# Kernel tuning notes

Hardware: AMD Instinct MI355X
Metric: run time of the kernel (lower is better)

## Reference

```python
import jax, jax.numpy as jnp
import numpy as np

N = 100_000      # nodes
E = 1_600_000    # edges (avg degree 16)
D_IN = 256
D_OUT = 128


def setup_inputs() -> dict:
    key = jax.random.key(0)
    ks = jax.random.split(key, 13)
    stdv = 1.0 / np.sqrt(D_OUT)      # matches reset_parameters
    std_att = 1.0                    # att_vec_* have fan 1 -> stdv 1
    std_av = 1.0 / np.sqrt(3.0)
    return {
        "x": jax.random.normal(ks[0], (N, D_IN), dtype=jnp.float32),
        "edge_src": jax.random.randint(ks[1], (E,), 0, N),
        "edge_dst": jax.random.randint(ks[2], (E,), 0, N),
        "w_low": jax.random.uniform(ks[3], (E,), dtype=jnp.float32) / 16.0,   # ~normalized adj
        "w_high": jax.random.normal(ks[4], (E,), dtype=jnp.float32) / 16.0,    # high-pass weights can be +/-
        "w_unnorm": jax.random.uniform(ks[5], (E,), dtype=jnp.float32),
        "W_low": jax.random.uniform(ks[6], (D_IN, D_OUT), jnp.float32, -stdv, stdv),
        "W_high": jax.random.uniform(ks[7], (D_IN, D_OUT), jnp.float32, -stdv, stdv),
        "W_mlp": jax.random.uniform(ks[8], (D_IN, D_OUT), jnp.float32, -stdv, stdv),
        "a_low": jax.random.uniform(ks[9], (D_OUT, 1), jnp.float32, -std_att, std_att),
        "a_high": jax.random.uniform(ks[10], (D_OUT, 1), jnp.float32, -std_att, std_att),
        "a_mlp": jax.random.uniform(ks[11], (D_OUT, 1), jnp.float32, -std_att, std_att),
        "att_vec": jax.random.uniform(ks[12], (3, 3), jnp.float32, -std_av, std_av),
    }


def _spmm(w, src, dst, h, n):
    # sparse [n,n] @ dense [n,d]: gather source rows, weight, scatter-add to dest
    return jax.ops.segment_sum(w[:, None] * h[src], dst, num_segments=n)


def reference(x, edge_src, edge_dst, w_low, w_high, w_unnorm,
              W_low, W_high, W_mlp, a_low, a_high, a_mlp, att_vec):
    n = x.shape[0]
    # variant=False path: relu(spmm(adj, x @ W))
    h_low = jax.nn.relu(_spmm(w_low, edge_src, edge_dst, x @ W_low, n))
    h_high = jax.nn.relu(_spmm(w_high, edge_src, edge_dst, x @ W_high, n))
    h_mlp = jax.nn.relu(x @ W_mlp)
    # attention3: sigmoid of per-branch scalar scores -> 3x3 mix -> softmax (T=3)
    scores = jnp.concatenate([h_low @ a_low, h_high @ a_high, h_mlp @ a_mlp], axis=1)  # [n,3]
    att = jax.nn.softmax((jax.nn.sigmoid(scores) @ att_vec) / 3.0, axis=1)
    return 3.0 * (att[:, 0:1] * h_low + att[:, 1:2] * h_high + att[:, 2:3] * h_mlp)
```

## Files before the change

kernel.cpp:

```cpp
#include <hip/hip_runtime.h>
#include <hip/hip_bf16.h>
#include <math.h>

#define D_IN   256
#define D_OUT  128
#define DZ     384

typedef __attribute__((ext_vector_type(8))) short short8;
typedef __attribute__((ext_vector_type(4))) float floatx4;

__device__ __forceinline__ unsigned short f2bf(float f) {
  union { float f; unsigned u; } v; v.f = f;
  unsigned r = v.u + 0x7fffu + ((v.u >> 16) & 1u);
  return (unsigned short)(r >> 16);
}

__global__ void prep_kernel(const float* __restrict__ Wl,
                            const float* __restrict__ Wh,
                            const float* __restrict__ Wm,
                            unsigned short* __restrict__ Bpack,
                            const float* __restrict__ x,
                            unsigned short* __restrict__ xb, int n8,
                            int* __restrict__ cnt, int n, int nxb) {
  int bid = blockIdx.x;
  if (bid < 384) {
    int t = bid * 256 + threadIdx.x;
    int j = t & 7;
    int lane = (t >> 3) & 63;
    int f = t >> 9;
    int nt = f % 24, kt = f / 24;
    int k = kt * 32 + (lane >> 4) * 8 + j;
    int n_ = nt * 16 + (lane & 15);
    const float* W = (n_ < 128) ? Wl : (n_ < 256 ? Wh : Wm);
    Bpack[t] = f2bf(W[k * D_OUT + (n_ & 127)]);
  } else if (bid < 384 + nxb) {
    int i = (bid - 384) * 256 + threadIdx.x;
    if (i < n8) {
      const float4* p = (const float4*)x + (size_t)i * 2;
      float4 f0 = p[0], f1 = p[1];
      short8 o;
      o[0] = (short)f2bf(f0.x); o[1] = (short)f2bf(f0.y);
      o[2] = (short)f2bf(f0.z); o[3] = (short)f2bf(f0.w);
      o[4] = (short)f2bf(f1.x); o[5] = (short)f2bf(f1.y);
      o[6] = (short)f2bf(f1.z); o[7] = (short)f2bf(f1.w);
      ((short8*)xb)[i] = o;
    }
  } else {
    int i = (bid - 384 - nxb) * 1024 + threadIdx.x * 4;
    if (i < n) *(int4*)&cnt[i] = make_int4(0, 0, 0, 0);
  }
}

#define LDSROW 392
__global__ __launch_bounds__(512, 4) void gemm_rank_kernel(
    const unsigned short* __restrict__ xb,
    const unsigned short* __restrict__ Bpack, unsigned short* __restrict__ Z,
    int n_nodes, const int* __restrict__ dst, int* __restrict__ cnt,
    int* __restrict__ rank, int E, int nrank) {
  __shared__ unsigned short tile[64 * LDSROW];
  const int bid = blockIdx.x;

  int gemm_id;
  if (bid < 2 * nrank) {
    if ((bid & 1) == 0) {
      int rb = bid >> 1;
      int e = (rb * 512 + threadIdx.x) * 4;
      if (e + 3 < E) {
        int4 d = *(const int4*)&dst[e];
        int r0 = atomicAdd(&cnt[d.x], 1);
        int r1 = atomicAdd(&cnt[d.y], 1);
        int r2 = atomicAdd(&cnt[d.z], 1);
        int r3 = atomicAdd(&cnt[d.w], 1);
        *(int4*)&rank[e] = make_int4(r0, r1, r2, r3);
      } else {
        for (int k = e; k < E; k++) rank[k] = atomicAdd(&cnt[dst[k]], 1);
      }
      return;
    }
    gemm_id = bid >> 1;
  } else {
    gemm_id = (bid - 2 * nrank) + nrank;
  }

  const int lane = threadIdx.x & 63;
  const int w = threadIdx.x >> 6;
  const int rowbase = gemm_id * 64;
  const int m16 = lane & 15, quad = lane >> 4;

  floatx4 acc[4][3];
#pragma unroll
  for (int s = 0; s < 4; s++)
#pragma unroll
    for (int c = 0; c < 3; c++) acc[s][c] = (floatx4)(0.f);

  const short8* xr[4];
#pragma unroll
  for (int s = 0; s < 4; s++) {
    int r = rowbase + s * 16 + m16;
    if (r > n_nodes - 1) r = n_nodes - 1;
    xr[s] = (const short8*)xb + (size_t)r * 32 + quad;
  }
  const short8* bp = (const short8*)Bpack + lane;

#pragma unroll
  for (int kt = 0; kt < 8; kt++) {
    short8 a[4];
#pragma unroll
    for (int s = 0; s < 4; s++) a[s] = xr[s][kt * 4];
#pragma unroll
    for (int c = 0; c < 3; c++) {
      short8 b = bp[(kt * 24 + w * 3 + c) * 64];
#pragma unroll
      for (int s = 0; s < 4; s++)
        acc[s][c] =
            __builtin_amdgcn_mfma_f32_16x16x32_bf16(a[s], b, acc[s][c], 0, 0, 0);
    }
  }

#pragma unroll
  for (int s = 0; s < 4; s++)
#pragma unroll
    for (int c = 0; c < 3; c++)
#pragma unroll
      for (int r = 0; r < 4; r++)
        tile[(s * 16 + quad * 4 + r) * LDSROW + (w * 3 + c) * 16 + m16] =
            f2bf(acc[s][c][r]);
  __syncthreads();

#pragma unroll
  for (int it = 0; it < 6; it++) {
    int chunk = it * 512 + threadIdx.x;
    int row = chunk / 48, col = (chunk % 48) * 8;
    int grow = rowbase + row;
    if (grow < n_nodes)
      *(short8*)(Z + (size_t)grow * DZ + col) =
          *(const short8*)&tile[row * LDSROW + col];
  }
}

__global__ __launch_bounds__(256) void scan1_kernel(
    const int* __restrict__ cnt, int* __restrict__ rowptr,
    int* __restrict__ bsum, int n) {
  __shared__ int sd[256];
  int t = threadIdx.x;
  int base = blockIdx.x * 1024 + t * 4;
  int v0 = base + 0 < n ? cnt[base + 0] : 0;
  int v1 = base + 1 < n ? cnt[base + 1] : 0;
  int v2 = base + 2 < n ? cnt[base + 2] : 0;
  int v3 = base + 3 < n ? cnt[base + 3] : 0;
  int tsum = v0 + v1 + v2 + v3;
  sd[t] = tsum;
  __syncthreads();
  for (int off = 1; off < 256; off <<= 1) {
    int add = (t >= off) ? sd[t - off] : 0;
    __syncthreads();
    sd[t] += add;
    __syncthreads();
  }
  int excl = sd[t] - tsum;
  if (base + 0 < n) rowptr[base + 0] = excl;
  if (base + 1 < n) rowptr[base + 1] = excl + v0;
  if (base + 2 < n) rowptr[base + 2] = excl + v0 + v1;
  if (base + 3 < n) rowptr[base + 3] = excl + v0 + v1 + v2;
  if (t == 255) bsum[blockIdx.x] = sd[255];
}

__global__ __launch_bounds__(128) void scan2_kernel(int* __restrict__ bsum,
                                                    int nb) {
  __shared__ int sd[128];
  int t = threadIdx.x;
  int v = t < nb ? bsum[t] : 0;
  sd[t] = v;
  __syncthreads();
  for (int off = 1; off < 128; off <<= 1) {
    int add = (t >= off) ? sd[t - off] : 0;
    __syncthreads();
    sd[t] += add;
    __syncthreads();
  }
  if (t < nb) bsum[t] = sd[t] - v;
}

__global__ void scan3_kernel(int* __restrict__ rowptr,
                             const int* __restrict__ bsum, int n, int E) {
  int i = blockIdx.x * 256 + threadIdx.x;
  if (i < n) {
    rowptr[i] = rowptr[i] + bsum[i >> 10];
    if (i == 0) rowptr[n] = E;
  }
}

__global__ void scatter_kernel(const int* __restrict__ src,
                               const int* __restrict__ dst,
                               const float* __restrict__ wlo,
                               const float* __restrict__ whi,
                               const int* __restrict__ rowptr,
                               const int* __restrict__ rank,
                               uint2* __restrict__ meta, int E) {
  int e = blockIdx.x * 256 + threadIdx.x;
  if (e < E) {
    int d = dst[e];
    int pos = rowptr[d] + rank[e];
    unsigned wl = f2bf(wlo[e]), wh = f2bf(whi[e]);
    meta[pos] = make_uint2((unsigned)src[e], wl | (wh << 16));
  }
}

__global__ __launch_bounds__(128) void node_kernel(
    const unsigned short* __restrict__ Zh, const int* __restrict__ rowptr,
    const uint2* __restrict__ meta, const float* __restrict__ a_low,
    const float* __restrict__ a_high, const float* __restrict__ a_mlp,
    const float* __restrict__ att_vec, float* __restrict__ out, int n_nodes) {
  int node = blockIdx.x * 2 + (threadIdx.x >> 6);
  if (node >= n_nodes) return;
  node = __builtin_amdgcn_readfirstlane(node);
  const int lane = threadIdx.x & 63;
  const int isHigh = lane >> 5;
  const int dbase = (lane & 31) * 4;
  const char* Zb = (const char*)Zh;

  const int start = rowptr[node];
  const int end = rowptr[node + 1];

  float acc0 = 0.f, acc1 = 0.f, acc2 = 0.f, acc3 = 0.f;
  auto wsel = [&](unsigned p) {
    return __uint_as_float(isHigh ? (p & 0xffff0000u) : (p << 16));
  };
  auto step = [&](uint2 z, float wv) {
    acc0 += wv * __uint_as_float(z.x << 16);
    acc1 += wv * __uint_as_float(z.x & 0xffff0000u);
    acc2 += wv * __uint_as_float(z.y << 16);
    acc3 += wv * __uint_as_float(z.y & 0xffff0000u);
  };

  int j = start;
  const int nfull = (end - start) & ~7;
  for (; j < start + nfull; j += 8) {
    uint2 m[8], z[8];
#pragma unroll
    for (int u = 0; u < 8; u++) m[u] = meta[j + u];
#pragma unroll
    for (int u = 0; u < 8; u++)
      z[u] = *(const uint2*)(Zb + (size_t)m[u].x * 768 + lane * 8);
#pragma unroll
    for (int u = 0; u < 8; u++) step(z[u], wsel(m[u].y));
  }
  for (; j < end; j++) {
    uint2 m0 = meta[j];
    uint2 z0 = *(const uint2*)(Zb + (size_t)m0.x * 768 + lane * 8);
    step(z0, wsel(m0.y));
  }

  float h0 = fmaxf(acc0, 0.f), h1 = fmaxf(acc1, 0.f);
  float h2 = fmaxf(acc2, 0.f), h3 = fmaxf(acc3, 0.f);

  uint2 zm =
      *(const uint2*)(Zb + (size_t)node * 768 + 512 + (size_t)(lane & 31) * 8);
  float q0 = fmaxf(__uint_as_float(zm.x << 16), 0.f);
  float q1 = fmaxf(__uint_as_float(zm.x & 0xffff0000u), 0.f);
  float q2 = fmaxf(__uint_as_float(zm.y << 16), 0.f);
  float q3 = fmaxf(__uint_as_float(zm.y & 0xffff0000u), 0.f);

  const float* av_b = isHigh ? a_high : a_low;
  float4 ab = *(const float4*)&av_b[dbase];
  float4 am = *(const float4*)&a_mlp[dbase];
  float v1 = h0 * ab.x + h1 * ab.y + h2 * ab.z + h3 * ab.w;
  float v2 = isHigh ? 0.f : (q0 * am.x + q1 * am.y + q2 * am.z + q3 * am.w);
#pragma unroll
  for (int off = 1; off < 32; off <<= 1) {
    v1 += __shfl_xor(v1, off);
    v2 += __shfl_xor(v2, off);
  }
  float s_lo = __shfl(v1, 0);
  float s_hi = __shfl(v1, 32);
  float s_ml = __shfl(v2, 0);

  float g0 = 1.f / (1.f + __expf(-s_lo));
  float g1 = 1.f / (1.f + __expf(-s_hi));
  float g2 = 1.f / (1.f + __expf(-s_ml));
  const float inv3 = 1.f / 3.f;
  float m0 = (g0 * att_vec[0] + g1 * att_vec[3] + g2 * att_vec[6]) * inv3;
  float m1 = (g0 * att_vec[1] + g1 * att_vec[4] + g2 * att_vec[7]) * inv3;
  float m2 = (g0 * att_vec[2] + g1 * att_vec[5] + g2 * att_vec[8]) * inv3;
  float mx = fmaxf(m0, fmaxf(m1, m2));
  float e0 = __expf(m0 - mx), e1 = __expf(m1 - mx), e2 = __expf(m2 - mx);
  float inv = 1.f / (e0 + e1 + e2);
  float c0 = 3.f * inv * e0, c1 = 3.f * inv * e1, c2 = 3.f * inv * e2;

  float hh0 = __shfl_xor(h0, 32);
  float hh1 = __shfl_xor(h1, 32);
  float hh2 = __shfl_xor(h2, 32);
  float hh3 = __shfl_xor(h3, 32);

  if (!isHigh) {
    float4 o;
    o.x = c0 * h0 + c1 * hh0 + c2 * q0;
    o.y = c0 * h1 + c1 * hh1 + c2 * q1;
    o.z = c0 * h2 + c1 * hh2 + c2 * q2;
    o.w = c0 * h3 + c1 * hh3 + c2 * q3;
    *(float4*)&out[(size_t)node * D_OUT + dbase] = o;
  }
}

extern "C" void kernel_launch(void* const* d_in, const int* in_sizes, int n_in,
                              void* d_out, int out_size, void* d_ws,
                              size_t ws_size, hipStream_t stream) {
  const float* x    = (const float*)d_in[0];
  const int*   esrc = (const int*)d_in[1];
  const int*   edst = (const int*)d_in[2];
  const float* wlo  = (const float*)d_in[3];
  const float* whi  = (const float*)d_in[4];
  const float* Wl   = (const float*)d_in[6];
  const float* Wh   = (const float*)d_in[7];
  const float* Wm   = (const float*)d_in[8];
  const float* alo  = (const float*)d_in[9];
  const float* ahi  = (const float*)d_in[10];
  const float* amlp = (const float*)d_in[11];
  const float* av   = (const float*)d_in[12];
  float* out = (float*)d_out;

  const int N = in_sizes[0] / D_IN;
  const int E = in_sizes[1];

  char* ws = (char*)d_ws;
  size_t off = 0;
  auto carve = [&](size_t bytes) -> void* {
    void* p = ws + off;
    off = (off + bytes + 255) & ~(size_t)255;
    return p;
  };
  unsigned short* Z     = (unsigned short*)carve((size_t)N * DZ * 2);
  unsigned short* xb    = (unsigned short*)carve((size_t)N * D_IN * 2);
  unsigned short* Bpack = (unsigned short*)carve(98304 * 2);
  int*   cnt    = (int*)carve((size_t)N * 4);
  int*   rowptr = (int*)carve((size_t)(N + 1) * 4);
  int*   rank   = (int*)carve((size_t)E * 4);
  int*   bsum   = (int*)carve(128 * 4);
  uint2* meta   = (uint2*)carve((size_t)E * 8);

  int n8 = in_sizes[0] / 8;
  int nxb = (n8 + 255) / 256;
  int nzb = (N + 1023) / 1024;
  prep_kernel<<<384 + nxb + nzb, 256, 0, stream>>>(Wl, Wh, Wm, Bpack, x, xb, n8,
                                                   cnt, N, nxb);

  int ngemm = (N + 63) / 64;
  int nrank = (E + 2047) / 2048;
  gemm_rank_kernel<<<ngemm + nrank, 512, 0, stream>>>(xb, Bpack, Z, N, edst,
                                                      cnt, rank, E, nrank);

  int nb = (N + 1023) / 1024;
  scan1_kernel<<<nb, 256, 0, stream>>>(cnt, rowptr, bsum, N);
  scan2_kernel<<<1, 128, 0, stream>>>(bsum, nb);
  scan3_kernel<<<(N + 255) / 256, 256, 0, stream>>>(rowptr, bsum, N, E);
  scatter_kernel<<<(E + 255) / 256, 256, 0, stream>>>(esrc, edst, wlo, whi,
                                                      rowptr, rank, meta, E);

  node_kernel<<<(N + 1) / 2, 128, 0, stream>>>(Z, rowptr, meta, alo, ahi, amlp,
                                               av, out, N);
}
```

Baseline: 468.7 us.

## Co-schedule rank counting with prep and edge scatter with GEMM

```diff
diff --git a/kernel.cpp b/kernel.cpp
--- a/kernel.cpp
+++ b/kernel.cpp
@@ -15,16 +15,41 @@
   return (unsigned short)(r >> 16);
 }
 
-__global__ void prep_kernel(const float* __restrict__ Wl,
-                            const float* __restrict__ Wh,
-                            const float* __restrict__ Wm,
-                            unsigned short* __restrict__ Bpack,
-                            const float* __restrict__ x,
-                            unsigned short* __restrict__ xb, int n8,
-                            int* __restrict__ cnt, int n, int nxb) {
-  int bid = blockIdx.x;
-  if (bid < 384) {
-    int t = bid * 256 + threadIdx.x;
+__global__ void prep_rank_kernel(const float* __restrict__ Wl,
+                                 const float* __restrict__ Wh,
+                                 const float* __restrict__ Wm,
+                                 unsigned short* __restrict__ Bpack,
+                                 const float* __restrict__ x,
+                                 unsigned short* __restrict__ xb, int n8,
+                                 const int* __restrict__ dst,
+                                 int* __restrict__ cnt, int* __restrict__ rank,
+                                 int E, int nrank) {
+  const int bid = blockIdx.x;
+  int prep_id;
+  if (bid < 2 * nrank) {
+    if ((bid & 1) == 0) {
+      int rb = bid >> 1;
+      int e = (rb * 256 + threadIdx.x) * 4;
+      if (e + 3 < E) {
+        int4 d = *(const int4*)&dst[e];
+        int r0 = atomicAdd(&cnt[d.x], 1);
+        int r1 = atomicAdd(&cnt[d.y], 1);
+        int r2 = atomicAdd(&cnt[d.z], 1);
+        int r3 = atomicAdd(&cnt[d.w], 1);
+        *(int4*)&rank[e] = make_int4(r0, r1, r2, r3);
+      } else {
+        for (int k = e; k < E && k >= 0; k++)
+          rank[k] = atomicAdd(&cnt[dst[k]], 1);
+      }
+      return;
+    }
+    prep_id = bid >> 1;
+  } else {
+    prep_id = bid - 2 * nrank + nrank;
+  }
+
+  if (prep_id < 384) {
+    int t = prep_id * 256 + threadIdx.x;
     int j = t & 7;
     int lane = (t >> 3) & 63;
     int f = t >> 9;
@@ -33,8 +58,8 @@
     int n_ = nt * 16 + (lane & 15);
     const float* W = (n_ < 128) ? Wl : (n_ < 256 ? Wh : Wm);
     Bpack[t] = f2bf(W[k * D_OUT + (n_ & 127)]);
-  } else if (bid < 384 + nxb) {
-    int i = (bid - 384) * 256 + threadIdx.x;
+  } else {
+    int i = (prep_id - 384) * 256 + threadIdx.x;
     if (i < n8) {
       const float4* p = (const float4*)x + (size_t)i * 2;
       float4 f0 = p[0], f1 = p[1];
@@ -45,96 +70,6 @@
       o[6] = (short)f2bf(f1.z); o[7] = (short)f2bf(f1.w);
       ((short8*)xb)[i] = o;
     }
-  } else {
-    int i = (bid - 384 - nxb) * 1024 + threadIdx.x * 4;
-    if (i < n) *(int4*)&cnt[i] = make_int4(0, 0, 0, 0);
-  }
-}
-
-#define LDSROW 392
-__global__ __launch_bounds__(512, 4) void gemm_rank_kernel(
-    const unsigned short* __restrict__ xb,
-    const unsigned short* __restrict__ Bpack, unsigned short* __restrict__ Z,
-    int n_nodes, const int* __restrict__ dst, int* __restrict__ cnt,
-    int* __restrict__ rank, int E, int nrank) {
-  __shared__ unsigned short tile[64 * LDSROW];
-  const int bid = blockIdx.x;
-
-  int gemm_id;
-  if (bid < 2 * nrank) {
-    if ((bid & 1) == 0) {
-      int rb = bid >> 1;
-      int e = (rb * 512 + threadIdx.x) * 4;
-      if (e + 3 < E) {
-        int4 d = *(const int4*)&dst[e];
-        int r0 = atomicAdd(&cnt[d.x], 1);
-        int r1 = atomicAdd(&cnt[d.y], 1);
-        int r2 = atomicAdd(&cnt[d.z], 1);
-        int r3 = atomicAdd(&cnt[d.w], 1);
-        *(int4*)&rank[e] = make_int4(r0, r1, r2, r3);
-      } else {
-        for (int k = e; k < E; k++) rank[k] = atomicAdd(&cnt[dst[k]], 1);
-      }
-      return;
-    }
-    gemm_id = bid >> 1;
-  } else {
-    gemm_id = (bid - 2 * nrank) + nrank;
-  }
-
-  const int lane = threadIdx.x & 63;
-  const int w = threadIdx.x >> 6;
-  const int rowbase = gemm_id * 64;
-  const int m16 = lane & 15, quad = lane >> 4;
-
-  floatx4 acc[4][3];
-#pragma unroll
-  for (int s = 0; s < 4; s++)
-#pragma unroll
-    for (int c = 0; c < 3; c++) acc[s][c] = (floatx4)(0.f);
-
-  const short8* xr[4];
-#pragma unroll
-  for (int s = 0; s < 4; s++) {
-    int r = rowbase + s * 16 + m16;
-    if (r > n_nodes - 1) r = n_nodes - 1;
-    xr[s] = (const short8*)xb + (size_t)r * 32 + quad;
-  }
-  const short8* bp = (const short8*)Bpack + lane;
-
-#pragma unroll
-  for (int kt = 0; kt < 8; kt++) {
-    short8 a[4];
-#pragma unroll
-    for (int s = 0; s < 4; s++) a[s] = xr[s][kt * 4];
-#pragma unroll
-    for (int c = 0; c < 3; c++) {
-      short8 b = bp[(kt * 24 + w * 3 + c) * 64];
-#pragma unroll
-      for (int s = 0; s < 4; s++)
-        acc[s][c] =
-            __builtin_amdgcn_mfma_f32_16x16x32_bf16(a[s], b, acc[s][c], 0, 0, 0);
-    }
-  }
-
-#pragma unroll
-  for (int s = 0; s < 4; s++)
-#pragma unroll
-    for (int c = 0; c < 3; c++)
-#pragma unroll
-      for (int r = 0; r < 4; r++)
-        tile[(s * 16 + quad * 4 + r) * LDSROW + (w * 3 + c) * 16 + m16] =
-            f2bf(acc[s][c][r]);
-  __syncthreads();
-
-#pragma unroll
-  for (int it = 0; it < 6; it++) {
-    int chunk = it * 512 + threadIdx.x;
-    int row = chunk / 48, col = (chunk % 48) * 8;
-    int grow = rowbase + row;
-    if (grow < n_nodes)
-      *(short8*)(Z + (size_t)grow * DZ + col) =
-          *(const short8*)&tile[row * LDSROW + col];
   }
 }
 
@@ -190,19 +125,103 @@
   }
 }
 
-__global__ void scatter_kernel(const int* __restrict__ src,
-                               const int* __restrict__ dst,
-                               const float* __restrict__ wlo,
-                               const float* __restrict__ whi,
-                               const int* __restrict__ rowptr,
-                               const int* __restrict__ rank,
-                               uint2* __restrict__ meta, int E) {
-  int e = blockIdx.x * 256 + threadIdx.x;
-  if (e < E) {
-    int d = dst[e];
-    int pos = rowptr[d] + rank[e];
-    unsigned wl = f2bf(wlo[e]), wh = f2bf(whi[e]);
-    meta[pos] = make_uint2((unsigned)src[e], wl | (wh << 16));
+#define LDSROW 392
+__global__ __launch_bounds__(512, 4) void gemm_scatter_kernel(
+    const unsigned short* __restrict__ xb,
+    const unsigned short* __restrict__ Bpack, unsigned short* __restrict__ Z,
+    int n_nodes, const int* __restrict__ src, const int* __restrict__ dst,
+    const float* __restrict__ wlo, const float* __restrict__ whi,
+    const int* __restrict__ rowptr, const int* __restrict__ rank,
+    uint2* __restrict__ meta, int E, int nscat) {
+  __shared__ unsigned short tile[64 * LDSROW];
+  const int bid = blockIdx.x;
+
+  int gemm_id;
+  if (bid < 2 * nscat) {
+    if ((bid & 1) == 0) {
+      int sb = bid >> 1;
+      int e = (sb * 512 + threadIdx.x) * 4;
+      if (e + 3 < E) {
+        int4 s4 = *(const int4*)&src[e];
+        int4 d4 = *(const int4*)&dst[e];
+        int4 r4 = *(const int4*)&rank[e];
+        float4 wl4 = *(const float4*)&wlo[e];
+        float4 wh4 = *(const float4*)&whi[e];
+        meta[rowptr[d4.x] + r4.x] =
+            make_uint2((unsigned)s4.x, f2bf(wl4.x) | ((unsigned)f2bf(wh4.x) << 16));
+        meta[rowptr[d4.y] + r4.y] =
+            make_uint2((unsigned)s4.y, f2bf(wl4.y) | ((unsigned)f2bf(wh4.y) << 16));
+        meta[rowptr[d4.z] + r4.z] =
+            make_uint2((unsigned)s4.z, f2bf(wl4.z) | ((unsigned)f2bf(wh4.z) << 16));
+        meta[rowptr[d4.w] + r4.w] =
+            make_uint2((unsigned)s4.w, f2bf(wl4.w) | ((unsigned)f2bf(wh4.w) << 16));
+      } else {
+        for (int k = e; k < E && k >= 0; k++) {
+          unsigned wl = f2bf(wlo[k]), wh = f2bf(whi[k]);
+          meta[rowptr[dst[k]] + rank[k]] =
+              make_uint2((unsigned)src[k], wl | (wh << 16));
+        }
+      }
+      return;
+    }
+    gemm_id = bid >> 1;
+  } else {
+    gemm_id = bid - 2 * nscat + nscat;
+  }
+
+  const int lane = threadIdx.x & 63;
+  const int w = threadIdx.x >> 6;
+  const int rowbase = gemm_id * 64;
+  const int m16 = lane & 15, quad = lane >> 4;
+
+  floatx4 acc[4][3];
+#pragma unroll
+  for (int s = 0; s < 4; s++)
+#pragma unroll
+    for (int c = 0; c < 3; c++) acc[s][c] = (floatx4)(0.f);
+
+  const short8* xr[4];
+#pragma unroll
+  for (int s = 0; s < 4; s++) {
+    int r = rowbase + s * 16 + m16;
+    if (r > n_nodes - 1) r = n_nodes - 1;
+    xr[s] = (const short8*)xb + (size_t)r * 32 + quad;
+  }
+  const short8* bp = (const short8*)Bpack + lane;
+
+#pragma unroll
+  for (int kt = 0; kt < 8; kt++) {
+    short8 a[4];
+#pragma unroll
+    for (int s = 0; s < 4; s++) a[s] = xr[s][kt * 4];
+#pragma unroll
+    for (int c = 0; c < 3; c++) {
+      short8 b = bp[(kt * 24 + w * 3 + c) * 64];
+#pragma unroll
+      for (int s = 0; s < 4; s++)
+        acc[s][c] =
+            __builtin_amdgcn_mfma_f32_16x16x32_bf16(a[s], b, acc[s][c], 0, 0, 0);
+    }
+  }
+
+#pragma unroll
+  for (int s = 0; s < 4; s++)
+#pragma unroll
+    for (int c = 0; c < 3; c++)
+#pragma unroll
+      for (int r = 0; r < 4; r++)
+        tile[(s * 16 + quad * 4 + r) * LDSROW + (w * 3 + c) * 16 + m16] =
+            f2bf(acc[s][c][r]);
+  __syncthreads();
+
+#pragma unroll
+  for (int it = 0; it < 6; it++) {
+    int chunk = it * 512 + threadIdx.x;
+    int row = chunk / 48, col = (chunk % 48) * 8;
+    int grow = rowbase + row;
+    if (grow < n_nodes)
+      *(short8*)(Z + (size_t)grow * DZ + col) =
+          *(const short8*)&tile[row * LDSROW + col];
   }
 }
 
@@ -340,21 +359,21 @@
 
   int n8 = in_sizes[0] / 8;
   int nxb = (n8 + 255) / 256;
-  int nzb = (N + 1023) / 1024;
-  prep_kernel<<<384 + nxb + nzb, 256, 0, stream>>>(Wl, Wh, Wm, Bpack, x, xb, n8,
-                                                   cnt, N, nxb);
-
-  int ngemm = (N + 63) / 64;
-  int nrank = (E + 2047) / 2048;
-  gemm_rank_kernel<<<ngemm + nrank, 512, 0, stream>>>(xb, Bpack, Z, N, edst,
-                                                      cnt, rank, E, nrank);
+
+  hipMemsetAsync(cnt, 0, (size_t)N * 4, stream);
+  int nrank = (E + 1023) / 1024;
+  prep_rank_kernel<<<384 + nxb + 2 * nrank - nrank, 256, 0, stream>>>(
+      Wl, Wh, Wm, Bpack, x, xb, n8, edst, cnt, rank, E, nrank);
 
   int nb = (N + 1023) / 1024;
   scan1_kernel<<<nb, 256, 0, stream>>>(cnt, rowptr, bsum, N);
   scan2_kernel<<<1, 128, 0, stream>>>(bsum, nb);
   scan3_kernel<<<(N + 255) / 256, 256, 0, stream>>>(rowptr, bsum, N, E);
-  scatter_kernel<<<(E + 255) / 256, 256, 0, stream>>>(esrc, edst, wlo, whi,
-                                                      rowptr, rank, meta, E);
+
+  int ngemm = (N + 63) / 64;
+  int nscat = (E + 2047) / 2048;
+  gemm_scatter_kernel<<<ngemm + nscat, 512, 0, stream>>>(
+      xb, Bpack, Z, N, esrc, edst, wlo, whi, rowptr, rank, meta, E, nscat);
 
   node_kernel<<<(N + 1) / 2, 128, 0, stream>>>(Z, rowptr, meta, alo, ahi, amlp,
                                                av, out, N);
```

Result: no change. 469.6 us (+0.2%).

## Replace atomic counting sort with two-level bucket sort for CSR build

Applied to the files above, without the earlier changes.

```diff
diff --git a/kernel.cpp b/kernel.cpp
--- a/kernel.cpp
+++ b/kernel.cpp
@@ -5,6 +5,7 @@
 #define D_IN   256
 #define D_OUT  128
 #define DZ     384
+#define NHB    256
 
 typedef __attribute__((ext_vector_type(8))) short short8;
 typedef __attribute__((ext_vector_type(4))) float floatx4;
@@ -15,26 +16,35 @@
   return (unsigned short)(r >> 16);
 }
 
-__global__ void prep_kernel(const float* __restrict__ Wl,
-                            const float* __restrict__ Wh,
-                            const float* __restrict__ Wm,
-                            unsigned short* __restrict__ Bpack,
-                            const float* __restrict__ x,
-                            unsigned short* __restrict__ xb, int n8,
-                            int* __restrict__ cnt, int n, int nxb) {
-  int bid = blockIdx.x;
-  if (bid < 384) {
-    int t = bid * 256 + threadIdx.x;
-    int j = t & 7;
-    int lane = (t >> 3) & 63;
-    int f = t >> 9;
+__global__ __launch_bounds__(256) void hist_prep_kernel(
+    const float* __restrict__ Wl, const float* __restrict__ Wh,
+    const float* __restrict__ Wm, unsigned short* __restrict__ Bpack,
+    const float* __restrict__ x, unsigned short* __restrict__ xb, int n8,
+    const int* __restrict__ dst, int* __restrict__ bh, int E, int NB1) {
+  __shared__ int hist[1024];
+  const int bid = blockIdx.x;
+  const int t = threadIdx.x;
+  if (bid < NHB) {
+    for (int k = t; k < NB1; k += 256) hist[k] = 0;
+    __syncthreads();
+    const int chunk = (E + NHB - 1) / NHB;
+    const int base = bid * chunk;
+    const int lim = min(E, base + chunk);
+    for (int e = base + t; e < lim; e += 256) atomicAdd(&hist[dst[e] >> 7], 1);
+    __syncthreads();
+    for (int k = t; k < NB1; k += 256) bh[k * NHB + bid] = hist[k];
+  } else if (bid < NHB + 384) {
+    int tt = (bid - NHB) * 256 + t;
+    int j = tt & 7;
+    int lane = (tt >> 3) & 63;
+    int f = tt >> 9;
     int nt = f % 24, kt = f / 24;
     int k = kt * 32 + (lane >> 4) * 8 + j;
     int n_ = nt * 16 + (lane & 15);
     const float* W = (n_ < 128) ? Wl : (n_ < 256 ? Wh : Wm);
-    Bpack[t] = f2bf(W[k * D_OUT + (n_ & 127)]);
-  } else if (bid < 384 + nxb) {
-    int i = (bid - 384) * 256 + threadIdx.x;
+    Bpack[tt] = f2bf(W[k * D_OUT + (n_ & 127)]);
+  } else {
+    int i = (bid - NHB - 384) * 256 + t;
     if (i < n8) {
       const float4* p = (const float4*)x + (size_t)i * 2;
       float4 f0 = p[0], f1 = p[1];
@@ -45,101 +55,11 @@
       o[6] = (short)f2bf(f1.z); o[7] = (short)f2bf(f1.w);
       ((short8*)xb)[i] = o;
     }
-  } else {
-    int i = (bid - 384 - nxb) * 1024 + threadIdx.x * 4;
-    if (i < n) *(int4*)&cnt[i] = make_int4(0, 0, 0, 0);
-  }
-}
-
-#define LDSROW 392
-__global__ __launch_bounds__(512, 4) void gemm_rank_kernel(
-    const unsigned short* __restrict__ xb,
-    const unsigned short* __restrict__ Bpack, unsigned short* __restrict__ Z,
-    int n_nodes, const int* __restrict__ dst, int* __restrict__ cnt,
-    int* __restrict__ rank, int E, int nrank) {
-  __shared__ unsigned short tile[64 * LDSROW];
-  const int bid = blockIdx.x;
-
-  int gemm_id;
-  if (bid < 2 * nrank) {
-    if ((bid & 1) == 0) {
-      int rb = bid >> 1;
-      int e = (rb * 512 + threadIdx.x) * 4;
-      if (e + 3 < E) {
-        int4 d = *(const int4*)&dst[e];
-        int r0 = atomicAdd(&cnt[d.x], 1);
-        int r1 = atomicAdd(&cnt[d.y], 1);
-        int r2 = atomicAdd(&cnt[d.z], 1);
-        int r3 = atomicAdd(&cnt[d.w], 1);
-        *(int4*)&rank[e] = make_int4(r0, r1, r2, r3);
-      } else {
-        for (int k = e; k < E; k++) rank[k] = atomicAdd(&cnt[dst[k]], 1);
-      }
-      return;
-    }
-    gemm_id = bid >> 1;
-  } else {
-    gemm_id = (bid - 2 * nrank) + nrank;
-  }
-
-  const int lane = threadIdx.x & 63;
-  const int w = threadIdx.x >> 6;
-  const int rowbase = gemm_id * 64;
-  const int m16 = lane & 15, quad = lane >> 4;
-
-  floatx4 acc[4][3];
-#pragma unroll
-  for (int s = 0; s < 4; s++)
-#pragma unroll
-    for (int c = 0; c < 3; c++) acc[s][c] = (floatx4)(0.f);
-
-  const short8* xr[4];
-#pragma unroll
-  for (int s = 0; s < 4; s++) {
-    int r = rowbase + s * 16 + m16;
-    if (r > n_nodes - 1) r = n_nodes - 1;
-    xr[s] = (const short8*)xb + (size_t)r * 32 + quad;
-  }
-  const short8* bp = (const short8*)Bpack + lane;
-
-#pragma unroll
-  for (int kt = 0; kt < 8; kt++) {
-    short8 a[4];
-#pragma unroll
-    for (int s = 0; s < 4; s++) a[s] = xr[s][kt * 4];
-#pragma unroll
-    for (int c = 0; c < 3; c++) {
-      short8 b = bp[(kt * 24 + w * 3 + c) * 64];
-#pragma unroll
-      for (int s = 0; s < 4; s++)
-        acc[s][c] =
-            __builtin_amdgcn_mfma_f32_16x16x32_bf16(a[s], b, acc[s][c], 0, 0, 0);
-    }
-  }
-
-#pragma unroll
-  for (int s = 0; s < 4; s++)
-#pragma unroll
-    for (int c = 0; c < 3; c++)
-#pragma unroll
-      for (int r = 0; r < 4; r++)
-        tile[(s * 16 + quad * 4 + r) * LDSROW + (w * 3 + c) * 16 + m16] =
-            f2bf(acc[s][c][r]);
-  __syncthreads();
-
-#pragma unroll
-  for (int it = 0; it < 6; it++) {
-    int chunk = it * 512 + threadIdx.x;
-    int row = chunk / 48, col = (chunk % 48) * 8;
-    int grow = rowbase + row;
-    if (grow < n_nodes)
-      *(short8*)(Z + (size_t)grow * DZ + col) =
-          *(const short8*)&tile[row * LDSROW + col];
   }
 }
 
 __global__ __launch_bounds__(256) void scan1_kernel(
-    const int* __restrict__ cnt, int* __restrict__ rowptr,
+    const int* __restrict__ cnt, int* __restrict__ outp,
     int* __restrict__ bsum, int n) {
   __shared__ int sd[256];
   int t = threadIdx.x;
@@ -158,51 +78,165 @@
     __syncthreads();
   }
   int excl = sd[t] - tsum;
-  if (base + 0 < n) rowptr[base + 0] = excl;
-  if (base + 1 < n) rowptr[base + 1] = excl + v0;
-  if (base + 2 < n) rowptr[base + 2] = excl + v0 + v1;
-  if (base + 3 < n) rowptr[base + 3] = excl + v0 + v1 + v2;
+  if (base + 0 < n) outp[base + 0] = excl;
+  if (base + 1 < n) outp[base + 1] = excl + v0;
+  if (base + 2 < n) outp[base + 2] = excl + v0 + v1;
+  if (base + 3 < n) outp[base + 3] = excl + v0 + v1 + v2;
   if (t == 255) bsum[blockIdx.x] = sd[255];
 }
 
-__global__ __launch_bounds__(128) void scan2_kernel(int* __restrict__ bsum,
+__global__ __launch_bounds__(256) void scan2_kernel(int* __restrict__ bsum,
                                                     int nb) {
-  __shared__ int sd[128];
+  __shared__ int sd[256];
   int t = threadIdx.x;
   int v = t < nb ? bsum[t] : 0;
   sd[t] = v;
   __syncthreads();
+  for (int off = 1; off < 256; off <<= 1) {
+    int add = (t >= off) ? sd[t - off] : 0;
+    __syncthreads();
+    sd[t] += add;
+    __syncthreads();
+  }
+  if (t < nb) bsum[t] = sd[t] - v;
+}
+
+__global__ void scan3_kernel(int* __restrict__ outp,
+                             const int* __restrict__ bsum, int n) {
+  int i = blockIdx.x * 256 + threadIdx.x;
+  if (i < n) outp[i] += bsum[i >> 10];
+}
+
+#define LDSROW 392
+__global__ __launch_bounds__(512, 4) void gemm_sort_kernel(
+    const unsigned short* __restrict__ xb,
+    const unsigned short* __restrict__ Bpack, unsigned short* __restrict__ Z,
+    int n_nodes, const int* __restrict__ src, const int* __restrict__ dst,
+    const float* __restrict__ wlo, const float* __restrict__ whi,
+    const int* __restrict__ bhscan, uint2* __restrict__ tmp, int E, int NB1) {
+  __shared__ unsigned short tile[64 * LDSROW];
+  const int bid = blockIdx.x;
+
+  int gemm_id;
+  if (bid < 2 * NHB) {
+    if ((bid & 1) == 0) {
+      int rb = bid >> 1;
+      int* cur = (int*)tile;
+      int t = threadIdx.x;
+      for (int k = t; k < NB1; k += 512) cur[k] = bhscan[k * NHB + rb];
+      __syncthreads();
+      const int chunk = (E + NHB - 1) / NHB;
+      const int base = rb * chunk;
+      const int lim = min(E, base + chunk);
+      for (int e = base + t; e < lim; e += 512) {
+        int d = dst[e];
+        int pos = atomicAdd(&cur[d >> 7], 1);
+        unsigned wl = f2bf(wlo[e]), wh = f2bf(whi[e]);
+        tmp[pos] = make_uint2((unsigned)src[e] | ((unsigned)(d & 127) << 20),
+                              wl | (wh << 16));
+      }
+      return;
+    }
+    gemm_id = bid >> 1;
+  } else {
+    gemm_id = bid - 2 * NHB + NHB;
+  }
+
+  const int lane = threadIdx.x & 63;
+  const int w = threadIdx.x >> 6;
+  const int rowbase = gemm_id * 64;
+  const int m16 = lane & 15, quad = lane >> 4;
+
+  floatx4 acc[4][3];
+#pragma unroll
+  for (int s = 0; s < 4; s++)
+#pragma unroll
+    for (int c = 0; c < 3; c++) acc[s][c] = (floatx4)(0.f);
+
+  const short8* xr[4];
+#pragma unroll
+  for (int s = 0; s < 4; s++) {
+    int r = rowbase + s * 16 + m16;
+    if (r > n_nodes - 1) r = n_nodes - 1;
+    xr[s] = (const short8*)xb + (size_t)r * 32 + quad;
+  }
+  const short8* bp = (const short8*)Bpack + lane;
+
+#pragma unroll
+  for (int kt = 0; kt < 8; kt++) {
+    short8 a[4];
+#pragma unroll
+    for (int s = 0; s < 4; s++) a[s] = xr[s][kt * 4];
+#pragma unroll
+    for (int c = 0; c < 3; c++) {
+      short8 b = bp[(kt * 24 + w * 3 + c) * 64];
+#pragma unroll
+      for (int s = 0; s < 4; s++)
+        acc[s][c] =
+            __builtin_amdgcn_mfma_f32_16x16x32_bf16(a[s], b, acc[s][c], 0, 0, 0);
+    }
+  }
+
+#pragma unroll
+  for (int s = 0; s < 4; s++)
+#pragma unroll
+    for (int c = 0; c < 3; c++)
+#pragma unroll
+      for (int r = 0; r < 4; r++)
+        tile[(s * 16 + quad * 4 + r) * LDSROW + (w * 3 + c) * 16 + m16] =
+            f2bf(acc[s][c][r]);
+  __syncthreads();
+
+#pragma unroll
+  for (int it = 0; it < 6; it++) {
+    int chunk = it * 512 + threadIdx.x;
+    int row = chunk / 48, col = (chunk % 48) * 8;
+    int grow = rowbase + row;
+    if (grow < n_nodes)
+      *(short8*)(Z + (size_t)grow * DZ + col) =
+          *(const short8*)&tile[row * LDSROW + col];
+  }
+}
+
+__global__ __launch_bounds__(256) void fine_kernel(
+    const uint2* __restrict__ tmp, const int* __restrict__ bhscan,
+    uint2* __restrict__ meta, int* __restrict__ rowptr, int NB1, int n, int E) {
+  __shared__ int fh[128];
+  __shared__ int sd[128];
+  __shared__ int cur[128];
+  const int b = blockIdx.x;
+  const int t = threadIdx.x;
+  const int s0 = bhscan[b * NHB];
+  const int s1 = (b == NB1 - 1) ? E : bhscan[(b + 1) * NHB];
+
+  if (t < 128) fh[t] = 0;
+  __syncthreads();
+  for (int i = s0 + t; i < s1; i += 256)
+    atomicAdd(&fh[(tmp[i].x >> 20) & 127], 1);
+  __syncthreads();
+
+  if (t < 128) sd[t] = fh[t];
+  __syncthreads();
   for (int off = 1; off < 128; off <<= 1) {
-    int add = (t >= off) ? sd[t - off] : 0;
-    __syncthreads();
-    sd[t] += add;
-    __syncthreads();
-  }
-  if (t < nb) bsum[t] = sd[t] - v;
-}
-
-__global__ void scan3_kernel(int* __restrict__ rowptr,
-                             const int* __restrict__ bsum, int n, int E) {
-  int i = blockIdx.x * 256 + threadIdx.x;
-  if (i < n) {
-    rowptr[i] = rowptr[i] + bsum[i >> 10];
-    if (i == 0) rowptr[n] = E;
-  }
-}
-
-__global__ void scatter_kernel(const int* __restrict__ src,
-                               const int* __restrict__ dst,
-                               const float* __restrict__ wlo,
-                               const float* __restrict__ whi,
-                               const int* __restrict__ rowptr,
-                               const int* __restrict__ rank,
-                               uint2* __restrict__ meta, int E) {
-  int e = blockIdx.x * 256 + threadIdx.x;
-  if (e < E) {
-    int d = dst[e];
-    int pos = rowptr[d] + rank[e];
-    unsigned wl = f2bf(wlo[e]), wh = f2bf(whi[e]);
-    meta[pos] = make_uint2((unsigned)src[e], wl | (wh << 16));
+    int add = (t >= off && t < 128) ? sd[t - off] : 0;
+    __syncthreads();
+    if (t < 128) sd[t] += add;
+    __syncthreads();
+  }
+  if (t < 128) {
+    int excl = sd[t] - fh[t];
+    cur[t] = excl;
+    int node = b * 128 + t;
+    if (node < n) rowptr[node] = s0 + excl;
+  }
+  if (b == 0 && t == 0) rowptr[n] = E;
+  __syncthreads();
+
+  for (int i = s0 + t; i < s1; i += 256) {
+    uint2 v = tmp[i];
+    int d = (v.x >> 20) & 127;
+    int pos = s0 + atomicAdd(&cur[d], 1);
+    meta[pos] = make_uint2(v.x & 0xFFFFFu, v.y);
   }
 }
 
@@ -321,6 +355,8 @@
 
   const int N = in_sizes[0] / D_IN;
   const int E = in_sizes[1];
+  const int NB1 = (N + 127) >> 7;
+  const int M = NB1 * NHB;
 
   char* ws = (char*)d_ws;
   size_t off = 0;
@@ -329,32 +365,32 @@
     off = (off + bytes + 255) & ~(size_t)255;
     return p;
   };
-  unsigned short* Z     = (unsigned short*)carve((size_t)N * DZ * 2);
-  unsigned short* xb    = (unsigned short*)carve((size_t)N * D_IN * 2);
-  unsigned short* Bpack = (unsigned short*)carve(98304 * 2);
-  int*   cnt    = (int*)carve((size_t)N * 4);
+  unsigned short* Z      = (unsigned short*)carve((size_t)N * DZ * 2);
+  unsigned short* xb     = (unsigned short*)carve((size_t)N * D_IN * 2);
+  unsigned short* Bpack  = (unsigned short*)carve(98304 * 2);
+  int*   bh     = (int*)carve((size_t)M * 4);
+  int*   bhscan = (int*)carve((size_t)M * 4);
+  int*   bsum   = (int*)carve(256 * 4);
   int*   rowptr = (int*)carve((size_t)(N + 1) * 4);
-  int*   rank   = (int*)carve((size_t)E * 4);
-  int*   bsum   = (int*)carve(128 * 4);
+  uint2* tmp    = (uint2*)carve((size_t)E * 8);
   uint2* meta   = (uint2*)carve((size_t)E * 8);
 
   int n8 = in_sizes[0] / 8;
   int nxb = (n8 + 255) / 256;
-  int nzb = (N + 1023) / 1024;
-  prep_kernel<<<384 + nxb + nzb, 256, 0, stream>>>(Wl, Wh, Wm, Bpack, x, xb, n8,
-                                                   cnt, N, nxb);
+
+  hist_prep_kernel<<<NHB + 384 + nxb, 256, 0, stream>>>(Wl, Wh, Wm, Bpack, x,
+                                                        xb, n8, edst, bh, E,
+                                                        NB1);
+  int nb1s = (M + 1023) / 1024;
+  scan1_kernel<<<nb1s, 256, 0, stream>>>(bh, bhscan, bsum, M);
+  scan2_kernel<<<1, 256, 0, stream>>>(bsum, nb1s);
+  scan3_kernel<<<(M + 255) / 256, 256, 0, stream>>>(bhscan, bsum, M);
 
   int ngemm = (N + 63) / 64;
-  int nrank = (E + 2047) / 2048;
-  gemm_rank_kernel<<<ngemm + nrank, 512, 0, stream>>>(xb, Bpack, Z, N, edst,
-                                                      cnt, rank, E, nrank);
-
-  int nb = (N + 1023) / 1024;
-  scan1_kernel<<<nb, 256, 0, stream>>>(cnt, rowptr, bsum, N);
-  scan2_kernel<<<1, 128, 0, stream>>>(bsum, nb);
-  scan3_kernel<<<(N + 255) / 256, 256, 0, stream>>>(rowptr, bsum, N, E);
-  scatter_kernel<<<(E + 255) / 256, 256, 0, stream>>>(esrc, edst, wlo, whi,
-                                                      rowptr, rank, meta, E);
+  gemm_sort_kernel<<<ngemm + NHB, 512, 0, stream>>>(
+      xb, Bpack, Z, N, esrc, edst, wlo, whi, bhscan, tmp, E, NB1);
+
+  fine_kernel<<<NB1, 256, 0, stream>>>(tmp, bhscan, meta, rowptr, NB1, N, E);
 
   node_kernel<<<(N + 1) / 2, 128, 0, stream>>>(Z, rowptr, meta, alo, ahi, amlp,
                                                av, out, N);
```

Result: faster. 451.2 us (-3.7%).
